# Kernel tuning notes

Measured on AMD Instinct MI355X. Metric: run time of the kernel, lower is better.

## Reference

```python
import jax, jax.numpy as jnp
import numpy as np

B, T, D, K = 8, 4096, 256, 8192

def setup_inputs() -> dict:
    key = jax.random.key(0)
    k1, k2 = jax.random.split(key)
    z = jax.random.normal(k1, (B, T, D), dtype=jnp.float32)
    codebook = jax.random.normal(k2, (K, D), dtype=jnp.float32)
    return {"z": z, "codebook": codebook}

def reference(z, codebook):
    Bm, Tm, Dm = z.shape
    z_flat = z.reshape(-1, Dm)                      # [N, D]
    z_norm_sq = jnp.sum(z_flat * z_flat, axis=1, keepdims=True)   # [N, 1]
    c_norm_sq = jnp.sum(codebook * codebook, axis=1)              # [K]
    dot = jnp.einsum('nd,kd->nk', z_flat, codebook)               # [N, K]
    distances = z_norm_sq + c_norm_sq - 2.0 * dot                 # [N, K]
    indices = jnp.argmin(distances, axis=-1)                      # [N]
    q_flat = codebook[indices]                                    # [N, D] gather
    q_z = q_flat.reshape(Bm, Tm, Dm)
    return q_z, indices.reshape(Bm, Tm)
```

## Files before the change

### kernel.cpp

```cpp
#include <hip/hip_runtime.h>
#include <hip/hip_bf16.h>

#define N_ROWS 32768
#define DDIM   256
#define KCODES 8192
#define QZ     (N_ROWS * DDIM)
#define NTILES 128
#define MARGIN 0.8f

typedef __attribute__((ext_vector_type(8))) short short8;
typedef __attribute__((ext_vector_type(4))) float f32x4;

__device__ __forceinline__ unsigned short f2bf(float f) {
  unsigned u = __builtin_bit_cast(unsigned, f);
  u += 0x7FFFu + ((u >> 16) & 1u);
  return (unsigned short)(u >> 16);
}

__device__ __forceinline__ void ins(float& b1, float& b2, float& b3, int& i1, int& i2,
                                    float d, int c) {
  bool l3 = d < b3, l2 = d < b2, l1 = d < b1;
  b3 = l3 ? (l2 ? b2 : d) : b3;
  b2 = l2 ? (l1 ? b1 : d) : b2;
  i2 = l2 ? (l1 ? i1 : c) : i2;
  b1 = l1 ? d : b1;
  i1 = l1 ? c : i1;
}

__device__ __forceinline__ void merge3(float& a1, float& a2, float& a3, int& x1, int& x2,
                                       float o1, float o2, float o3, int y1, int y2) {
  bool oW = o1 < a1;
  float mx1 = oW ? a1 : o1;  int mxi = oW ? x1 : y1;
  float n1  = oW ? o1 : a1;  int ni1 = oW ? y1 : x1;
  bool lA = a2 < o2;
  float lo2 = lA ? a2 : o2;  int li2 = lA ? x2 : y2;
  float hi2 = lA ? o2 : a2;
  bool m2w = mx1 < lo2;
  float n2 = m2w ? mx1 : lo2; int ni2 = m2w ? mxi : li2;
  float n3 = fminf(fminf(fmaxf(mx1, lo2), hi2), fminf(a3, o3));
  a1 = n1; a2 = n2; a3 = n3; x1 = ni1; x2 = ni2;
}

__global__ __launch_bounds__(256) void vq_cnorm(const float* __restrict__ cb,
                                                float* __restrict__ cn) {
  int n = blockIdx.x * 4 + (threadIdx.x >> 6);
  int lane = threadIdx.x & 63;
  float4 c4 = *reinterpret_cast<const float4*>(cb + (size_t)n * DDIM + lane * 4);
  double s = (double)c4.x * c4.x + (double)c4.y * c4.y +
             (double)c4.z * c4.z + (double)c4.w * c4.w;
  #pragma unroll
  for (int off = 32; off > 0; off >>= 1) s += __shfl_down(s, off, 64);
  if (lane == 0) cn[n] = (float)s;
}

__global__ __launch_bounds__(256) void vq_prep(const float* __restrict__ cb,
                                               unsigned char* __restrict__ wcb,
                                               float* __restrict__ cn) {
  int n = blockIdx.x * 4 + (threadIdx.x >> 6);
  int lane = threadIdx.x & 63;
  float4 c4 = *reinterpret_cast<const float4*>(cb + (size_t)n * DDIM + lane * 4);
  double s = (double)c4.x * c4.x + (double)c4.y * c4.y +
             (double)c4.z * c4.z + (double)c4.w * c4.w;
  #pragma unroll
  for (int off = 32; off > 0; off >>= 1) s += __shfl_down(s, off, 64);
  if (lane == 0) cn[n] = (float)s;

  unsigned short h0 = f2bf(c4.x), h1 = f2bf(c4.y), h2 = f2bf(c4.z), h3 = f2bf(c4.w);
  size_t base = (size_t)n * 512 +
                (size_t)((((lane >> 1) ^ (n & 7)) << 4) + (lane & 1) * 8);
  *reinterpret_cast<ushort4*>(wcb + base) = make_ushort4(h0, h1, h2, h3);
}

__global__ __launch_bounds__(256, 2) void vq_mfma(
    const float* __restrict__ z, const unsigned char* __restrict__ wcb,
    const float* __restrict__ cn, const float* __restrict__ cb,
    float* __restrict__ out,
    int* __restrict__ cntA, int4* __restrict__ rowsA,
    int* __restrict__ cntB, int* __restrict__ rowsB) {
  __shared__ __align__(16) unsigned char cs[2][32768];
  __shared__ float rb1[2][64], rb2[2][64], rb3[2][64];
  __shared__ int   ri1[2][64], ri2[2][64];
  __shared__ int   sIdx[64];

  const int tid = threadIdx.x;
  const int w = tid >> 6, lane = tid & 63;
  const int wm = w >> 1, wn = w & 1;
  const int g = lane >> 4, l15 = lane & 15;

  short8 zh[2][8];
  const int rA = blockIdx.x * 64 + wm * 32 + l15;
  #pragma unroll
  for (int mf = 0; mf < 2; ++mf) {
    #pragma unroll
    for (int dc = 0; dc < 8; ++dc) {
      const float* zp = z + (size_t)(rA + mf * 16) * DDIM + dc * 32 + g * 8;
      float4 f0 = *reinterpret_cast<const float4*>(zp);
      float4 f1 = *reinterpret_cast<const float4*>(zp + 4);
      short8 hh;
      hh[0] = (short)f2bf(f0.x); hh[1] = (short)f2bf(f0.y);
      hh[2] = (short)f2bf(f0.z); hh[3] = (short)f2bf(f0.w);
      hh[4] = (short)f2bf(f1.x); hh[5] = (short)f2bf(f1.y);
      hh[6] = (short)f2bf(f1.z); hh[7] = (short)f2bf(f1.w);
      zh[mf][dc] = hh;
    }
  }

  float b1[8], b2[8], b3[8];
  int i1[8], i2[8];
  #pragma unroll
  for (int s = 0; s < 8; ++s) { b1[s] = 3.4e38f; b2[s] = 3.4e38f; b3[s] = 3.4e38f; i1[s] = 0; i2[s] = 0; }

  #pragma unroll
  for (int i = 0; i < 8; ++i) {
    __builtin_amdgcn_global_load_lds(
        (const __attribute__((address_space(1))) void*)(wcb + tid * 16 + i * 4096),
        (__attribute__((address_space(3))) void*)(&cs[0][tid * 16 + i * 4096]), 16, 0, 0);
  }
  __syncthreads();

  const int cc0 = wn * 32 + l15;
  const int cc1 = cc0 + 16;
  const int swz = cc0 & 7;

  for (int nt = 0; nt < NTILES; ++nt) {
    const int cur = nt & 1;
    if (nt + 1 < NTILES) {
      const unsigned char* gsrc = wcb + (size_t)(nt + 1) * 32768;
      #pragma unroll
      for (int i = 0; i < 8; ++i) {
        __builtin_amdgcn_global_load_lds(
            (const __attribute__((address_space(1))) void*)(gsrc + tid * 16 + i * 4096),
            (__attribute__((address_space(3))) void*)(&cs[cur ^ 1][tid * 16 + i * 4096]), 16, 0, 0);
      }
    }

    int code0 = nt * 64 + cc0;
    float cn0 = cn[code0];
    float cn1 = cn[code0 + 16];

    const unsigned char* lb = cs[cur];
    f32x4 a00 = {0.f, 0.f, 0.f, 0.f}, a01 = a00, a10 = a00, a11 = a00;
    #pragma unroll
    for (int dc = 0; dc < 8; ++dc) {
      int u = dc * 4 + g;
      int o0 = cc0 * 512 + ((u ^ swz) << 4);
      int o1 = cc1 * 512 + ((u ^ swz) << 4);
      short8 c0 = *reinterpret_cast<const short8*>(lb + o0);
      short8 c1 = *reinterpret_cast<const short8*>(lb + o1);
      a00 = __builtin_amdgcn_mfma_f32_16x16x32_bf16(zh[0][dc], c0, a00, 0, 0, 0);
      a01 = __builtin_amdgcn_mfma_f32_16x16x32_bf16(zh[0][dc], c1, a01, 0, 0, 0);
      a10 = __builtin_amdgcn_mfma_f32_16x16x32_bf16(zh[1][dc], c0, a10, 0, 0, 0);
      a11 = __builtin_amdgcn_mfma_f32_16x16x32_bf16(zh[1][dc], c1, a11, 0, 0, 0);
    }

    #pragma unroll
    for (int mf = 0; mf < 2; ++mf) {
      const f32x4 an0 = mf ? a10 : a00;
      const f32x4 an1 = mf ? a11 : a01;
      #pragma unroll
      for (int r = 0; r < 4; ++r) {
        const int s = mf * 4 + r;
        float d0 = fmaf(-2.0f, an0[r], cn0);
        ins(b1[s], b2[s], b3[s], i1[s], i2[s], d0, code0);
        float d1 = fmaf(-2.0f, an1[r], cn1);
        ins(b1[s], b2[s], b3[s], i1[s], i2[s], d1, code0 + 16);
      }
    }
    __syncthreads();
  }

  #pragma unroll
  for (int s = 0; s < 8; ++s) {
    float B1 = b1[s], B2 = b2[s], B3 = b3[s];
    int I1 = i1[s], I2 = i2[s];
    #pragma unroll
    for (int m = 1; m <= 8; m <<= 1) {
      float o1 = __shfl_xor(B1, m, 64), o2 = __shfl_xor(B2, m, 64), o3 = __shfl_xor(B3, m, 64);
      int y1 = __shfl_xor(I1, m, 64), y2 = __shfl_xor(I2, m, 64);
      merge3(B1, B2, B3, I1, I2, o1, o2, o3, y1, y2);
    }
    if (l15 == 0) {
      int row = wm * 32 + (s >> 2) * 16 + g * 4 + (s & 3);
      rb1[wn][row] = B1; rb2[wn][row] = B2; rb3[wn][row] = B3;
      ri1[wn][row] = I1; ri2[wn][row] = I2;
    }
  }
  __syncthreads();

  if (tid < 64) {
    float B1 = rb1[0][tid], B2 = rb2[0][tid], B3 = rb3[0][tid];
    int I1 = ri1[0][tid], I2 = ri2[0][tid];
    merge3(B1, B2, B3, I1, I2, rb1[1][tid], rb2[1][tid], rb3[1][tid], ri1[1][tid], ri2[1][tid]);
    int grow = blockIdx.x * 64 + tid;
    out[QZ + grow] = (float)I1;
    sIdx[tid] = I1;
    if (B3 - B1 < MARGIN) {
      int p = atomicAdd(cntB, 1);
      rowsB[p] = grow;
    } else if (B2 - B1 < MARGIN) {
      int p = atomicAdd(cntA, 1);
      rowsA[p] = make_int4(grow, I1, I2, 0);
    }
  }
  __syncthreads();

  #pragma unroll
  for (int i = 0; i < 16; ++i) {
    int f = tid + i * 256;
    int r = f >> 6, c4i = f & 63;
    float4 v = *reinterpret_cast<const float4*>(cb + (size_t)sIdx[r] * DDIM + c4i * 4);
    *reinterpret_cast<float4*>(&out[(size_t)(blockIdx.x * 64 + r) * DDIM + c4i * 4]) = v;
  }
}

__global__ __launch_bounds__(256) void vq_pairs(
    const float* __restrict__ z, const float* __restrict__ cb, const float* __restrict__ cn,
    float* __restrict__ out, const int* __restrict__ cntA, const int4* __restrict__ rowsA) {
  int n = *cntA;
  int lane = threadIdx.x & 63;
  for (int e = blockIdx.x * 4 + (threadIdx.x >> 6); e < n; e += gridDim.x * 4) {
    int4 ent = rowsA[e];
    int row = ent.x, c1 = ent.y, c2 = ent.z;
    float4 zv = *reinterpret_cast<const float4*>(z + (size_t)row * DDIM + lane * 4);
    float4 a = *reinterpret_cast<const float4*>(cb + (size_t)c1 * DDIM + lane * 4);
    float4 b = *reinterpret_cast<const float4*>(cb + (size_t)c2 * DDIM + lane * 4);
    float p1 = zv.x * a.x + zv.y * a.y + zv.z * a.z + zv.w * a.w;
    float p2 = zv.x * b.x + zv.y * b.y + zv.z * b.z + zv.w * b.w;
    #pragma unroll
    for (int m = 1; m <= 32; m <<= 1) { p1 += __shfl_xor(p1, m, 64); p2 += __shfl_xor(p2, m, 64); }
    float d1 = cn[c1] - 2.0f * p1;
    float d2 = cn[c2] - 2.0f * p2;
    int win = (d2 < d1 || (d2 == d1 && c2 < c1)) ? c2 : c1;
    if (lane == 0) out[QZ + row] = (float)win;
    float4 cw = *reinterpret_cast<const float4*>(cb + (size_t)win * DDIM + lane * 4);
    *reinterpret_cast<float4*>(&out[(size_t)row * DDIM + lane * 4]) = cw;
  }
}

#define FS_CODES 128
#define FS_PAD   257
__global__ __launch_bounds__(256) void vq_fullsweep(
    const float* __restrict__ z, const float* __restrict__ cb, const float* __restrict__ cn,
    const int* __restrict__ cntB, const int* __restrict__ rowsB,
    unsigned long long* __restrict__ keysB) {
  __shared__ float csL[FS_CODES * FS_PAD];
  __shared__ float zr[DDIM];
  __shared__ float part[4][FS_CODES];
  const int nB = *cntB;
  if (nB == 0) return;
  const int cid = blockIdx.x & 63;
  const int sid = blockIdx.x >> 6;
  const int t = threadIdx.x;
  const int q = t >> 6, k = t & 63;

  const float* src = cb + (size_t)cid * FS_CODES * DDIM;
  #pragma unroll
  for (int i = 0; i < 32; ++i) {
    int f = t + i * 256;
    int code = f >> 6, j = f & 63;
    float4 v = *reinterpret_cast<const float4*>(src + (size_t)f * 4);
    *reinterpret_cast<float4*>(&csL[code * FS_PAD + j * 4]) = v;
  }
  float cnk = (t < FS_CODES) ? cn[cid * FS_CODES + t] : 0.f;

  for (int r = sid; r < nB; r += 4) {
    const int row = rowsB[r];
    __syncthreads();
    if (t < 64)
      *reinterpret_cast<float4*>(&zr[t * 4]) =
          *reinterpret_cast<const float4*>(z + (size_t)row * DDIM + t * 4);
    __syncthreads();

    float acc0 = 0.f, acc1 = 0.f;
    #pragma unroll
    for (int j = 0; j < 16; ++j) {
      float4 a  = *reinterpret_cast<const float4*>(&zr[q * 64 + j * 4]);
      float4 c0 = *reinterpret_cast<const float4*>(&csL[k * FS_PAD + q * 64 + j * 4]);
      float4 c1 = *reinterpret_cast<const float4*>(&csL[(k + 64) * FS_PAD + q * 64 + j * 4]);
      acc0 = fmaf(a.x, c0.x, acc0); acc0 = fmaf(a.y, c0.y, acc0);
      acc0 = fmaf(a.z, c0.z, acc0); acc0 = fmaf(a.w, c0.w, acc0);
      acc1 = fmaf(a.x, c1.x, acc1); acc1 = fmaf(a.y, c1.y, acc1);
      acc1 = fmaf(a.z, c1.z, acc1); acc1 = fmaf(a.w, c1.w, acc1);
    }
    part[q][k] = acc0;
    part[q][k + 64] = acc1;
    __syncthreads();

    if (t < FS_CODES) {
      float dot = part[0][t] + part[1][t] + part[2][t] + part[3][t];
      float d = cnk - 2.0f * dot;
      int code = cid * FS_CODES + t;
      unsigned m = __builtin_bit_cast(unsigned, d);
      m = (m >> 31) ? ~m : (m | 0x80000000u);
      unsigned long long key = ((unsigned long long)m << 32) | (unsigned)code;
      #pragma unroll
      for (int mm = 1; mm <= 32; mm <<= 1) {
        unsigned long long o = __shfl_xor(key, mm, 64);
        key = (o < key) ? o : key;
      }
      if (k == 0) atomicMin(&keysB[r], key);
    }
  }
}

__global__ __launch_bounds__(256) void vq_finishB(
    const float* __restrict__ cb, float* __restrict__ out,
    const int* __restrict__ cntB, const int* __restrict__ rowsB,
    const unsigned long long* __restrict__ keysB) {
  int nB = *cntB;
  int lane = threadIdx.x & 63;
  for (int e = blockIdx.x * 4 + (threadIdx.x >> 6); e < nB; e += gridDim.x * 4) {
    int row = rowsB[e];
    int idx = (int)(keysB[e] & 0xFFFFFFFFULL);
    if (lane == 0) out[QZ + row] = (float)idx;
    *reinterpret_cast<float4*>(&out[(size_t)row * DDIM + lane * 4]) =
        *reinterpret_cast<const float4*>(cb + (size_t)idx * DDIM + lane * 4);
  }
}

#define FB_BM 64
#define FB_BK 32
#define FB_LD 260
__global__ __launch_bounds__(256) void vq_main_fb(const float* __restrict__ z,
                                                  const float* __restrict__ cb,
                                                  const float* __restrict__ cn,
                                                  float* __restrict__ out) {
  __shared__ float zs[FB_BM * FB_LD];
  __shared__ float csh[FB_BK * FB_LD];
  __shared__ float redd[FB_BM][16];
  __shared__ int   redi[FB_BM][16];
  __shared__ int   sidx[FB_BM];
  const int t = threadIdx.x;
  const int row0 = blockIdx.x * FB_BM;
  #pragma unroll
  for (int i = 0; i < 16; ++i) {
    int f = t + i * 256; int r = f >> 6, c4 = f & 63;
    *reinterpret_cast<float4*>(&zs[r * FB_LD + c4 * 4]) =
        *reinterpret_cast<const float4*>(z + (size_t)(row0 + r) * DDIM + c4 * 4);
  }
  const int tr = t >> 4, tc = t & 15;
  float best[4]; int bidx[4];
  #pragma unroll
  for (int i = 0; i < 4; ++i) { best[i] = 3.4e38f; bidx[i] = 0; }
  for (int kt = 0; kt < KCODES; kt += FB_BK) {
    __syncthreads();
    #pragma unroll
    for (int i = 0; i < 8; ++i) {
      int f = t + i * 256; int r = f >> 6, c4 = f & 63;
      *reinterpret_cast<float4*>(&csh[r * FB_LD + c4 * 4]) =
          *reinterpret_cast<const float4*>(cb + (size_t)(kt + r) * DDIM + c4 * 4);
    }
    __syncthreads();
    float acc[4][2] = {{0.f,0.f},{0.f,0.f},{0.f,0.f},{0.f,0.f}};
    #pragma unroll 8
    for (int d4 = 0; d4 < 64; ++d4) {
      float4 b0 = *reinterpret_cast<const float4*>(&csh[tc * FB_LD + d4 * 4]);
      float4 b1v = *reinterpret_cast<const float4*>(&csh[(tc + 16) * FB_LD + d4 * 4]);
      #pragma unroll
      for (int i = 0; i < 4; ++i) {
        float4 a = *reinterpret_cast<const float4*>(&zs[(4 * tr + i) * FB_LD + d4 * 4]);
        acc[i][0] = fmaf(a.x, b0.x, acc[i][0]); acc[i][0] = fmaf(a.y, b0.y, acc[i][0]);
        acc[i][0] = fmaf(a.z, b0.z, acc[i][0]); acc[i][0] = fmaf(a.w, b0.w, acc[i][0]);
        acc[i][1] = fmaf(a.x, b1v.x, acc[i][1]); acc[i][1] = fmaf(a.y, b1v.y, acc[i][1]);
        acc[i][1] = fmaf(a.z, b1v.z, acc[i][1]); acc[i][1] = fmaf(a.w, b1v.w, acc[i][1]);
      }
    }
    float cn0 = cn[kt + tc], cn1 = cn[kt + tc + 16];
    #pragma unroll
    for (int i = 0; i < 4; ++i) {
      float d0 = cn0 - 2.0f * acc[i][0];
      if (d0 < best[i]) { best[i] = d0; bidx[i] = kt + tc; }
      float d1 = cn1 - 2.0f * acc[i][1];
      if (d1 < best[i]) { best[i] = d1; bidx[i] = kt + tc + 16; }
    }
  }
  #pragma unroll
  for (int i = 0; i < 4; ++i) { redd[4 * tr + i][tc] = best[i]; redi[4 * tr + i][tc] = bidx[i]; }
  __syncthreads();
  if (t < FB_BM) {
    float bd = redd[t][0]; int bi = redi[t][0];
    #pragma unroll
    for (int j = 1; j < 16; ++j) {
      float d = redd[t][j]; int ix = redi[t][j];
      if (d < bd || (d == bd && ix < bi)) { bd = d; bi = ix; }
    }
    sidx[t] = bi;
    out[QZ + row0 + t] = (float)bi;
  }
  __syncthreads();
  #pragma unroll
  for (int i = 0; i < 16; ++i) {
    int f = t + i * 256; int r = f >> 6, c4 = f & 63;
    *reinterpret_cast<float4*>(&out[(size_t)(row0 + r) * DDIM + c4 * 4]) =
        *reinterpret_cast<const float4*>(cb + (size_t)sidx[r] * DDIM + c4 * 4);
  }
}

extern "C" void kernel_launch(void* const* d_in, const int* in_sizes, int n_in,
                              void* d_out, int out_size, void* d_ws, size_t ws_size,
                              hipStream_t stream) {
  const float* z  = (const float*)d_in[0];
  const float* cb = (const float*)d_in[1];
  float* out = (float*)d_out;

  const size_t OFF_CN   = (size_t)KCODES * 512;
  const size_t OFF_CNT  = OFF_CN + (size_t)KCODES * 4;
  const size_t OFF_RA   = OFF_CNT + 16;
  const size_t OFF_RB   = OFF_RA + (size_t)N_ROWS * 16;
  const size_t OFF_KEYS = OFF_RB + (size_t)N_ROWS * 4;
  const size_t NEED     = OFF_KEYS + (size_t)N_ROWS * 8;

  if (ws_size >= NEED) {
    unsigned char* wcb = (unsigned char*)d_ws;
    float* cn = (float*)(wcb + OFF_CN);
    int* cntA = (int*)(wcb + OFF_CNT);
    int* cntB = (int*)(wcb + OFF_CNT + 4);
    int4* rowsA = (int4*)(wcb + OFF_RA);
    int* rowsB = (int*)(wcb + OFF_RB);
    unsigned long long* keysB = (unsigned long long*)(wcb + OFF_KEYS);
    hipMemsetAsync(cntA, 0, 8, stream);
    hipMemsetAsync(keysB, 0xFF, (size_t)N_ROWS * 8, stream);
    vq_prep<<<KCODES / 4, 256, 0, stream>>>(cb, wcb, cn);
    vq_mfma<<<N_ROWS / 64, 256, 0, stream>>>(z, wcb, cn, cb, out,
                                             cntA, rowsA, cntB, rowsB);
    vq_pairs<<<128, 256, 0, stream>>>(z, cb, cn, out, cntA, rowsA);
    vq_fullsweep<<<256, 256, 0, stream>>>(z, cb, cn, cntB, rowsB, keysB);
    vq_finishB<<<64, 256, 0, stream>>>(cb, out, cntB, rowsB, keysB);
  } else {
    float* cn = (float*)d_ws;
    vq_cnorm<<<KCODES / 4, 256, 0, stream>>>(cb, cn);
    vq_main_fb<<<N_ROWS / FB_BM, 256, 0, stream>>>(z, cb, cn, out);
  }
}
```

Baseline: 476.3 us.

## Restructure codebook tile layout, pipeline loads with vmcnt waits, widen fallback grids

Packs each 64-code bf16 tile together with its norms into one contiguous block with a new unswizzled layout, so the code norms are read from LDS instead of global memory. The main loop issues the next tile's async loads first, waits only on the previous tile's loads via explicit vmcnt counts, and uses raw barriers instead of __syncthreads. The top-3 insert uses med3/min instructions. Separately, the pairs and fullsweep fallback kernels get larger grids, and fullsweep blocks with no rows exit early. The removed swizzle may bring back LDS bank conflicts, and the hand-counted vmcnt values must match the number of outstanding loads exactly.

```diff
diff --git a/kernel.cpp b/kernel.cpp
--- a/kernel.cpp
+++ b/kernel.cpp
@@ -5,11 +5,16 @@
 #define DDIM   256
 #define KCODES 8192
 #define QZ     (N_ROWS * DDIM)
-#define NTILES 128
+#define NT64   128
+#define TBYTES 33792
 #define MARGIN 0.8f
 
 typedef __attribute__((ext_vector_type(8))) short short8;
 typedef __attribute__((ext_vector_type(4))) float f32x4;
+
+#define AS1 __attribute__((address_space(1)))
+#define AS3 __attribute__((address_space(3)))
+#define VMW(n) asm volatile("s_waitcnt vmcnt(" #n ")" ::: "memory")
 
 __device__ __forceinline__ unsigned short f2bf(float f) {
   unsigned u = __builtin_bit_cast(unsigned, f);
@@ -19,12 +24,13 @@
 
 __device__ __forceinline__ void ins(float& b1, float& b2, float& b3, int& i1, int& i2,
                                     float d, int c) {
-  bool l3 = d < b3, l2 = d < b2, l1 = d < b1;
-  b3 = l3 ? (l2 ? b2 : d) : b3;
-  b2 = l2 ? (l1 ? b1 : d) : b2;
+  bool l1 = d < b1, l2 = d < b2;
+  float nb1 = fminf(d, b1);
+  float nb2 = __builtin_amdgcn_fmed3f(b1, b2, d);
+  float nb3 = __builtin_amdgcn_fmed3f(b2, b3, d);
   i2 = l2 ? (l1 ? i1 : c) : i2;
-  b1 = l1 ? d : b1;
   i1 = l1 ? c : i1;
+  b1 = nb1; b2 = nb2; b3 = nb3;
 }
 
 __device__ __forceinline__ void merge3(float& a1, float& a2, float& a3, int& x1, int& x2,
@@ -66,25 +72,28 @@
   if (lane == 0) cn[n] = (float)s;
 
   unsigned short h0 = f2bf(c4.x), h1 = f2bf(c4.y), h2 = f2bf(c4.z), h3 = f2bf(c4.w);
-  size_t base = (size_t)n * 512 +
-                (size_t)((((lane >> 1) ^ (n & 7)) << 4) + (lane & 1) * 8);
+  int T = n >> 6, c = n & 63, gi = c >> 4, ci = c & 15;
+  size_t tb = (size_t)T * TBYTES;
+  size_t base = tb + (size_t)gi * 8192 + (size_t)(lane >> 1) * 256 +
+                (size_t)ci * 16 + (size_t)(lane & 1) * 8;
   *reinterpret_cast<ushort4*>(wcb + base) = make_ushort4(h0, h1, h2, h3);
+  if (lane == 0)
+    *reinterpret_cast<float*>(wcb + tb + 32768 + (size_t)c * 4) = (float)s;
 }
 
 __global__ __launch_bounds__(256, 2) void vq_mfma(
     const float* __restrict__ z, const unsigned char* __restrict__ wcb,
-    const float* __restrict__ cn, const float* __restrict__ cb,
-    float* __restrict__ out,
+    const float* __restrict__ cb, float* __restrict__ out,
     int* __restrict__ cntA, int4* __restrict__ rowsA,
     int* __restrict__ cntB, int* __restrict__ rowsB) {
-  __shared__ __align__(16) unsigned char cs[2][32768];
+  __shared__ __align__(16) unsigned char cs[2][TBYTES];
   __shared__ float rb1[2][64], rb2[2][64], rb3[2][64];
   __shared__ int   ri1[2][64], ri2[2][64];
   __shared__ int   sIdx[64];
 
   const int tid = threadIdx.x;
   const int w = tid >> 6, lane = tid & 63;
-  const int wm = w >> 1, wn = w & 1;
+  const int wm = w >> 1, wh = w & 1;
   const int g = lane >> 4, l15 = lane & 15;
 
   short8 zh[2][8];
@@ -110,49 +119,47 @@
   #pragma unroll
   for (int s = 0; s < 8; ++s) { b1[s] = 3.4e38f; b2[s] = 3.4e38f; b3[s] = 3.4e38f; i1[s] = 0; i2[s] = 0; }
 
-  #pragma unroll
-  for (int i = 0; i < 8; ++i) {
-    __builtin_amdgcn_global_load_lds(
-        (const __attribute__((address_space(1))) void*)(wcb + tid * 16 + i * 4096),
-        (__attribute__((address_space(3))) void*)(&cs[0][tid * 16 + i * 4096]), 16, 0, 0);
-  }
-  __syncthreads();
-
-  const int cc0 = wn * 32 + l15;
-  const int cc1 = cc0 + 16;
-  const int swz = cc0 & 7;
-
-  for (int nt = 0; nt < NTILES; ++nt) {
-    const int cur = nt & 1;
-    if (nt + 1 < NTILES) {
-      const unsigned char* gsrc = wcb + (size_t)(nt + 1) * 32768;
-      #pragma unroll
-      for (int i = 0; i < 8; ++i) {
-        __builtin_amdgcn_global_load_lds(
-            (const __attribute__((address_space(1))) void*)(gsrc + tid * 16 + i * 4096),
-            (__attribute__((address_space(3))) void*)(&cs[cur ^ 1][tid * 16 + i * 4096]), 16, 0, 0);
-      }
-    }
-
-    int code0 = nt * 64 + cc0;
-    float cn0 = cn[code0];
-    float cn1 = cn[code0 + 16];
-
-    const unsigned char* lb = cs[cur];
+#define STAGE(T_, S_) do {                                                      \
+    const unsigned char* gs_ = wcb + (size_t)(T_) * TBYTES + (size_t)w * 8192;  \
+    _Pragma("unroll")                                                           \
+    for (int r_ = 0; r_ < 8; ++r_)                                              \
+      __builtin_amdgcn_global_load_lds(                                         \
+          (const AS1 void*)(gs_ + r_ * 1024 + lane * 16),                       \
+          (AS3 void*)(&cs[S_][w * 8192 + r_ * 1024 + lane * 16]), 16, 0, 0);    \
+    if (w == 0)                                                                 \
+      __builtin_amdgcn_global_load_lds(                                         \
+          (const AS1 void*)(wcb + (size_t)(T_) * TBYTES + 32768 + lane * 16),   \
+          (AS3 void*)(&cs[S_][32768 + lane * 16]), 16, 0, 0);                   \
+  } while (0)
+
+  STAGE(0, 0);
+  const int gi0 = wh * 2, gi1 = wh * 2 + 1;
+
+  for (int t = 0; t < NT64; ++t) {
+    if (t + 1 < NT64) {
+      STAGE(t + 1, (t + 1) & 1);
+      if (w == 0) { VMW(9); } else { VMW(8); }
+    } else {
+      VMW(0);
+    }
+    __builtin_amdgcn_s_barrier();
+
+    const unsigned char* lb = cs[t & 1];
+    float cn0 = *reinterpret_cast<const float*>(lb + 32768 + (wh * 32 + l15) * 4);
+    float cn1 = *reinterpret_cast<const float*>(lb + 32768 + (wh * 32 + 16 + l15) * 4);
     f32x4 a00 = {0.f, 0.f, 0.f, 0.f}, a01 = a00, a10 = a00, a11 = a00;
     #pragma unroll
     for (int dc = 0; dc < 8; ++dc) {
-      int u = dc * 4 + g;
-      int o0 = cc0 * 512 + ((u ^ swz) << 4);
-      int o1 = cc1 * 512 + ((u ^ swz) << 4);
-      short8 c0 = *reinterpret_cast<const short8*>(lb + o0);
-      short8 c1 = *reinterpret_cast<const short8*>(lb + o1);
+      int uo = (dc * 4 + g) * 256 + l15 * 16;
+      short8 c0 = *reinterpret_cast<const short8*>(lb + gi0 * 8192 + uo);
+      short8 c1 = *reinterpret_cast<const short8*>(lb + gi1 * 8192 + uo);
       a00 = __builtin_amdgcn_mfma_f32_16x16x32_bf16(zh[0][dc], c0, a00, 0, 0, 0);
+      a10 = __builtin_amdgcn_mfma_f32_16x16x32_bf16(zh[1][dc], c0, a10, 0, 0, 0);
       a01 = __builtin_amdgcn_mfma_f32_16x16x32_bf16(zh[0][dc], c1, a01, 0, 0, 0);
-      a10 = __builtin_amdgcn_mfma_f32_16x16x32_bf16(zh[1][dc], c0, a10, 0, 0, 0);
       a11 = __builtin_amdgcn_mfma_f32_16x16x32_bf16(zh[1][dc], c1, a11, 0, 0, 0);
     }
 
+    int code0 = t * 64 + wh * 32 + l15;
     #pragma unroll
     for (int mf = 0; mf < 2; ++mf) {
       const f32x4 an0 = mf ? a10 : a00;
@@ -166,8 +173,9 @@
         ins(b1[s], b2[s], b3[s], i1[s], i2[s], d1, code0 + 16);
       }
     }
-    __syncthreads();
-  }
+    __builtin_amdgcn_s_barrier();
+  }
+#undef STAGE
 
   #pragma unroll
   for (int s = 0; s < 8; ++s) {
@@ -181,8 +189,8 @@
     }
     if (l15 == 0) {
       int row = wm * 32 + (s >> 2) * 16 + g * 4 + (s & 3);
-      rb1[wn][row] = B1; rb2[wn][row] = B2; rb3[wn][row] = B3;
-      ri1[wn][row] = I1; ri2[wn][row] = I2;
+      rb1[wh][row] = B1; rb2[wh][row] = B2; rb3[wh][row] = B3;
+      ri1[wh][row] = I1; ri2[wh][row] = I2;
     }
   }
   __syncthreads();
@@ -252,6 +260,7 @@
   const int sid = blockIdx.x >> 6;
   const int t = threadIdx.x;
   const int q = t >> 6, k = t & 63;
+  if (sid >= nB && sid > 0) return;
 
   const float* src = cb + (size_t)cid * FS_CODES * DDIM;
   #pragma unroll
@@ -263,7 +272,7 @@
   }
   float cnk = (t < FS_CODES) ? cn[cid * FS_CODES + t] : 0.f;
 
-  for (int r = sid; r < nB; r += 4) {
+  for (int r = sid; r < nB; r += 16) {
     const int row = rowsB[r];
     __syncthreads();
     if (t < 64)
@@ -403,7 +412,7 @@
   const float* cb = (const float*)d_in[1];
   float* out = (float*)d_out;
 
-  const size_t OFF_CN   = (size_t)KCODES * 512;
+  const size_t OFF_CN   = (size_t)NT64 * TBYTES;
   const size_t OFF_CNT  = OFF_CN + (size_t)KCODES * 4;
   const size_t OFF_RA   = OFF_CNT + 16;
   const size_t OFF_RB   = OFF_RA + (size_t)N_ROWS * 16;
@@ -421,10 +430,10 @@
     hipMemsetAsync(cntA, 0, 8, stream);
     hipMemsetAsync(keysB, 0xFF, (size_t)N_ROWS * 8, stream);
     vq_prep<<<KCODES / 4, 256, 0, stream>>>(cb, wcb, cn);
-    vq_mfma<<<N_ROWS / 64, 256, 0, stream>>>(z, wcb, cn, cb, out,
+    vq_mfma<<<N_ROWS / 64, 256, 0, stream>>>(z, wcb, cb, out,
                                              cntA, rowsA, cntB, rowsB);
-    vq_pairs<<<128, 256, 0, stream>>>(z, cb, cn, out, cntA, rowsA);
-    vq_fullsweep<<<256, 256, 0, stream>>>(z, cb, cn, cntB, rowsB, keysB);
+    vq_pairs<<<256, 256, 0, stream>>>(z, cb, cn, out, cntA, rowsA);
+    vq_fullsweep<<<1024, 256, 0, stream>>>(z, cb, cn, cntB, rowsB, keysB);
     vq_finishB<<<64, 256, 0, stream>>>(cb, out, cntB, rowsB, keysB);
   } else {
     float* cn = (float*)d_ws;
```

Measured after the change: 457.8 us. 1.04x faster.
